# Performance work log

Measured on AMD Instinct MI355X. Metric: run time of the kernel, lower is better.

The kernel has to match this reference:

```python
import jax, jax.numpy as jnp
import numpy as np

B, L, H, W, C = 2, 32, 16, 16, 32  # L must equal channels for the view() to be consistent
CH = L  # conv channel count


def setup_inputs() -> dict:
    key = jax.random.key(0)
    k1, k2, k3, k4, k5 = jax.random.split(key, 5)
    return {
        "inputs": jax.random.normal(k1, (B, L, H, W, C), dtype=jnp.float32),
        "W1": jax.random.normal(k2, (CH // 2, CH), dtype=jnp.float32) * 0.1,
        "b1": jax.random.normal(k3, (CH // 2,), dtype=jnp.float32) * 0.1,
        "W2": jax.random.normal(k4, (CH, CH), dtype=jnp.float32) * 0.1,
        "b2": jax.random.normal(k5, (CH,), dtype=jnp.float32) * 0.1,
        "gamma": jnp.ones((1,), dtype=jnp.float32),
    }


def reference(inputs, W1, b1, W2, b2, gamma):
    b, l, h, w, c = inputs.shape
    n = l * h * w  # flattened 'spatial' positions after the (buggy-but-faithful) reshape
    # conv1x1 over dim-1 (torch Conv3d treats dim-1 as channels)
    x1 = jnp.einsum('ol,blhwc->bohwc', W1, inputs) + b1[None, :, None, None, None]
    # permute (0,4,1,2,3) then view(b, c//2, l*h*w)
    x1 = jnp.transpose(x1, (0, 4, 1, 2, 3)).reshape(b, c // 2, n)
    # attn[b, i, j] = sum_k x1[b, k, i] * x1[b, k, j]; softmax over last dim
    attn = jax.nn.softmax(jnp.einsum('bki,bkj->bij', x1, x1), axis=-1)  # [b, n, n]
    x2 = jnp.einsum('ol,blhwc->bohwc', W2, inputs) + b2[None, :, None, None, None]
    x2 = jnp.transpose(x2, (0, 4, 1, 2, 3)).reshape(b, c, n)
    # x2 @ attn^T : out[b, c, i] = sum_j x2[b, c, j] * attn[b, i, j]
    out = jnp.einsum('bcj,bij->bci', x2, attn)
    out = jnp.transpose(out.reshape(b, c, l, h, w), (0, 2, 3, 4, 1))
    return out * gamma + inputs
```

## Files before the change

kernel.cpp:

```cpp
#include <hip/hip_runtime.h>
#include <hip/hip_bf16.h>
#include <math.h>

typedef __bf16 bf16x8 __attribute__((ext_vector_type(8)));
typedef __bf16 bf16x4v __attribute__((ext_vector_type(4)));
typedef short  s16x4  __attribute__((ext_vector_type(4)));
typedef float  floatx16 __attribute__((ext_vector_type(16)));

#define KQ_ELEMS (2 * 8192 * 16)
#define OACC_OFF 1572864
#define ACC_FLOATS (16384 * 32 + 16384)
#define SQRT_LOG2E 1.2011224087864498f
#define LSPLIT 4

__global__ __launch_bounds__(256) void proj_kernel(
    const float* __restrict__ in, const float* __restrict__ W1,
    const float* __restrict__ b1, const float* __restrict__ W2,
    const float* __restrict__ b2,
    __hip_bfloat16* __restrict__ Kq, __hip_bfloat16* __restrict__ Vswz,
    float* __restrict__ acc0)
{
    __shared__ float Xs[32][32];
    __shared__ float W1s[16 * 32];
    __shared__ float W2s[32 * 32];
    const int t = threadIdx.x;
    const int bid = blockIdx.x;
    const int b = bid >> 8;
    const int hw = bid & 255;

    {
        int gid = bid * 256 + t;
        *(float4*)(acc0 + (size_t)gid * 4) = make_float4(0.f, 0.f, 0.f, 0.f);
        if (gid < 4096)
            *(float4*)(acc0 + 524288 + (size_t)gid * 4) = make_float4(0.f, 0.f, 0.f, 0.f);
    }

    {
        int l = t >> 3, cs = (t & 7) * 4;
        float4 v = *(const float4*)(in + (((size_t)b * 32 + l) * 256 + hw) * 32 + cs);
        *(float4*)&Xs[l][cs] = v;
    }
    if (t < 128) *(float4*)&W1s[t * 4] = *(const float4*)(W1 + t * 4);
    *(float4*)&W2s[t * 4] = *(const float4*)(W2 + t * 4);
    __syncthreads();

    const int c = t & 31;
    const int g = t >> 5;

#pragma unroll
    for (int oo = 0; oo < 2; ++oo) {
        int o = g * 2 + oo;
        float acc = b1[o];
#pragma unroll
        for (int l = 0; l < 32; ++l) acc += W1s[o * 32 + l] * Xs[l][c];
        int k = c >> 1;
        int i = (c & 1) * 4096 + o * 256 + hw;
        Kq[((size_t)b * 8192 + i) * 16 + k] = __float2bfloat16(acc * SQRT_LOG2E);
    }
#pragma unroll
    for (int oo = 0; oo < 4; ++oo) {
        int o = g * 4 + oo;
        float acc = b2[o];
#pragma unroll
        for (int l = 0; l < 32; ++l) acc += W2s[o * 32 + l] * Xs[l][c];
        int j = o * 256 + hw;
        int jt = j >> 5, rem = j & 31;
        int gg = rem >> 3, h = (rem >> 2) & 1, idx = rem & 3;
        Vswz[(size_t)b * 262144 + jt * 1024 + gg * 256 + h * 128 + c * 4 + idx] =
            __float2bfloat16(acc);
    }
}

__global__ __launch_bounds__(256) void flash_kernel(
    const __hip_bfloat16* __restrict__ Kq, const __hip_bfloat16* __restrict__ Vswz,
    float* __restrict__ Oacc, float* __restrict__ Lacc)
{
    const int t = threadIdx.x;
    const int lane = t & 63;
    const int wv = t >> 6;
    const int m = lane & 31;
    const int h = lane >> 5;

    const int bid = blockIdx.x;
    const int s = bid & 15;
    const int itile = (bid >> LSPLIT) & 63;
    const int b = bid >> (LSPLIT + 6);
    const int i0 = itile * 128 + wv * 32;
    const int niter = 512 >> 5;
    const int jt0 = s * niter;

    const __hip_bfloat16* Kb = Kq + (size_t)b * 8192 * 16;
    const __hip_bfloat16* Vb = Vswz + (size_t)b * 262144 + h * 128 + m * 4;

    const bf16x8 bq = *(const bf16x8*)(Kb + (size_t)(i0 + m) * 16 + h * 8);

    floatx16 oa = {}, ob = {};
    float2 l01 = {0.f, 0.f}, l23 = {0.f, 0.f};

    bf16x8 ak = *(const bf16x8*)(Kb + (size_t)(jt0 * 32 + m) * 16 + h * 8);
    s16x4 vf0 = *(const s16x4*)(Vb + (size_t)jt0 * 1024 + 0);
    s16x4 vf1 = *(const s16x4*)(Vb + (size_t)jt0 * 1024 + 256);
    s16x4 vf2 = *(const s16x4*)(Vb + (size_t)jt0 * 1024 + 512);
    s16x4 vf3 = *(const s16x4*)(Vb + (size_t)jt0 * 1024 + 768);

    for (int it = 0; it < niter; ++it) {
        const int jtn = jt0 + (it + 1 < niter ? it + 1 : it);
        bf16x8 ak_n = *(const bf16x8*)(Kb + (size_t)(jtn * 32 + m) * 16 + h * 8);
        s16x4 vn0 = *(const s16x4*)(Vb + (size_t)jtn * 1024 + 0);
        s16x4 vn1 = *(const s16x4*)(Vb + (size_t)jtn * 1024 + 256);
        s16x4 vn2 = *(const s16x4*)(Vb + (size_t)jtn * 1024 + 512);
        s16x4 vn3 = *(const s16x4*)(Vb + (size_t)jtn * 1024 + 768);

        floatx16 sc = __builtin_amdgcn_mfma_f32_32x32x16_bf16(ak, bq, (floatx16){}, 0, 0, 0);

#pragma unroll
        for (int g = 0; g < 4; ++g) {
            bf16x4v pb;
            float e0 = __builtin_amdgcn_exp2f(sc[4 * g + 0]);
            float e1 = __builtin_amdgcn_exp2f(sc[4 * g + 1]);
            float e2 = __builtin_amdgcn_exp2f(sc[4 * g + 2]);
            float e3 = __builtin_amdgcn_exp2f(sc[4 * g + 3]);
            l01.x += e0; l01.y += e1; l23.x += e2; l23.y += e3;
            pb[0] = (__bf16)e0; pb[1] = (__bf16)e1; pb[2] = (__bf16)e2; pb[3] = (__bf16)e3;
            s16x4 vf = (g == 0) ? vf0 : (g == 1) ? vf1 : (g == 2) ? vf2 : vf3;
            if (g < 2)
                oa = __builtin_amdgcn_mfma_f32_32x32x8bf16_1k(
                         __builtin_bit_cast(s16x4, pb), vf, oa, 0, 0, 0);
            else
                ob = __builtin_amdgcn_mfma_f32_32x32x8bf16_1k(
                         __builtin_bit_cast(s16x4, pb), vf, ob, 0, 0, 0);
        }
        ak = ak_n; vf0 = vn0; vf1 = vn1; vf2 = vn2; vf3 = vn3;
    }

    oa = oa + ob;
    float l = (l01.x + l01.y) + (l23.x + l23.y);
    l += __shfl_xor(l, 32);

#pragma unroll
    for (int r = 0; r < 16; ++r) {
        int iloc = (r & 3) + 8 * (r >> 2) + 4 * h;
        size_t row = (size_t)b * 8192 + i0 + iloc;
        unsafeAtomicAdd(&Oacc[row * 32 + m], oa[r]);
    }
    if (h == 0)
        unsafeAtomicAdd(&Lacc[(size_t)b * 8192 + i0 + m], l);
}

__global__ __launch_bounds__(256) void finalize_kernel(
    const float* __restrict__ Oacc, const float* __restrict__ Lacc,
    const float* __restrict__ in, const float* __restrict__ gamma,
    float* __restrict__ out)
{
    const int t = threadIdx.x;
    const int c = t & 31;
    const size_t row = (size_t)blockIdx.x * 8 + (t >> 5);
    size_t idx = row * 32 + c;
    out[idx] = (Oacc[idx] / Lacc[row]) * gamma[0] + in[idx];
}

extern "C" void kernel_launch(void* const* d_in, const int* in_sizes, int n_in,
                              void* d_out, int out_size, void* d_ws, size_t ws_size,
                              hipStream_t stream) {
    const float* in = (const float*)d_in[0];
    const float* W1 = (const float*)d_in[1];
    const float* b1 = (const float*)d_in[2];
    const float* W2 = (const float*)d_in[3];
    const float* b2 = (const float*)d_in[4];
    const float* gamma = (const float*)d_in[5];
    float* out = (float*)d_out;

    __hip_bfloat16* Kq = (__hip_bfloat16*)d_ws;
    __hip_bfloat16* Vswz = Kq + KQ_ELEMS;
    float* Oacc = (float*)((char*)d_ws + OACC_OFF);
    float* Lacc = Oacc + 16384 * 32;

    proj_kernel<<<512, 256, 0, stream>>>(in, W1, b1, W2, b2, Kq, Vswz, Oacc);
    flash_kernel<<<2 * 64 * (1 << LSPLIT), 256, 0, stream>>>(Kq, Vswz, Oacc, Lacc);
    finalize_kernel<<<2048, 256, 0, stream>>>(Oacc, Lacc, in, gamma, out);
}
```

Before: 112.3 us.

## Compute softmax row sums via MFMA with ones, halve key split, unroll by two

The softmax denominator is now accumulated by an extra MFMA that multiplies the bf16 probabilities by a ones matrix, replacing per-lane scalar adds and a cross-lane shuffle. The key-dimension split drops from 16 to 8 chunks, so each block iterates longer and issues fewer atomics. The loop is unrolled by two with double-buffered fragment loads, fp32-to-bf16 conversion uses a packed builtin when the compiler provides one, and occupancy is hinted via launch bounds. The extra MFMA per group adds matrix-unit work, and the row sums now come from bf16-rounded probabilities, which slightly changes numerics.

Measured after the change: 117.8 us. 4.9% more time.

```diff
diff --git a/kernel.cpp b/kernel.cpp
--- a/kernel.cpp
+++ b/kernel.cpp
@@ -3,15 +3,15 @@
 #include <math.h>
 
 typedef __bf16 bf16x8 __attribute__((ext_vector_type(8)));
-typedef __bf16 bf16x4v __attribute__((ext_vector_type(4)));
+typedef __bf16 bf16x2 __attribute__((ext_vector_type(2)));
+typedef short  s16x2  __attribute__((ext_vector_type(2)));
 typedef short  s16x4  __attribute__((ext_vector_type(4)));
 typedef float  floatx16 __attribute__((ext_vector_type(16)));
 
 #define KQ_ELEMS (2 * 8192 * 16)
 #define OACC_OFF 1572864
-#define ACC_FLOATS (16384 * 32 + 16384)
 #define SQRT_LOG2E 1.2011224087864498f
-#define LSPLIT 4
+#define LSPLIT 3
 
 __global__ __launch_bounds__(256) void proj_kernel(
     const float* __restrict__ in, const float* __restrict__ W1,
@@ -71,7 +71,9 @@
     }
 }
 
-__global__ __launch_bounds__(256) void flash_kernel(
+struct Frags { bf16x8 ak; s16x4 v0, v1, v2, v3; };
+
+__global__ __launch_bounds__(256, 4) void flash_kernel(
     const __hip_bfloat16* __restrict__ Kq, const __hip_bfloat16* __restrict__ Vswz,
     float* __restrict__ Oacc, float* __restrict__ Lacc)
 {
@@ -82,60 +84,69 @@
     const int h = lane >> 5;
 
     const int bid = blockIdx.x;
-    const int s = bid & 15;
+    const int s = bid & ((1 << LSPLIT) - 1);
     const int itile = (bid >> LSPLIT) & 63;
     const int b = bid >> (LSPLIT + 6);
     const int i0 = itile * 128 + wv * 32;
-    const int niter = 512 >> 5;
+    const int niter = (8192 >> LSPLIT) >> 5;
     const int jt0 = s * niter;
 
     const __hip_bfloat16* Kb = Kq + (size_t)b * 8192 * 16;
     const __hip_bfloat16* Vb = Vswz + (size_t)b * 262144 + h * 128 + m * 4;
 
     const bf16x8 bq = *(const bf16x8*)(Kb + (size_t)(i0 + m) * 16 + h * 8);
+    const s16x4 vones = {(short)0x3F80, (short)0x3F80, (short)0x3F80, (short)0x3F80};
 
-    floatx16 oa = {}, ob = {};
-    float2 l01 = {0.f, 0.f}, l23 = {0.f, 0.f};
+    floatx16 oa = {}, ob = {}, lacc = {};
 
-    bf16x8 ak = *(const bf16x8*)(Kb + (size_t)(jt0 * 32 + m) * 16 + h * 8);
-    s16x4 vf0 = *(const s16x4*)(Vb + (size_t)jt0 * 1024 + 0);
-    s16x4 vf1 = *(const s16x4*)(Vb + (size_t)jt0 * 1024 + 256);
-    s16x4 vf2 = *(const s16x4*)(Vb + (size_t)jt0 * 1024 + 512);
-    s16x4 vf3 = *(const s16x4*)(Vb + (size_t)jt0 * 1024 + 768);
+    auto load = [&](int jt) {
+        Frags f;
+        f.ak = *(const bf16x8*)(Kb + (size_t)(jt * 32 + m) * 16 + h * 8);
+        f.v0 = *(const s16x4*)(Vb + (size_t)jt * 1024 + 0);
+        f.v1 = *(const s16x4*)(Vb + (size_t)jt * 1024 + 256);
+        f.v2 = *(const s16x4*)(Vb + (size_t)jt * 1024 + 512);
+        f.v3 = *(const s16x4*)(Vb + (size_t)jt * 1024 + 768);
+        return f;
+    };
 
-    for (int it = 0; it < niter; ++it) {
-        const int jtn = jt0 + (it + 1 < niter ? it + 1 : it);
-        bf16x8 ak_n = *(const bf16x8*)(Kb + (size_t)(jtn * 32 + m) * 16 + h * 8);
-        s16x4 vn0 = *(const s16x4*)(Vb + (size_t)jtn * 1024 + 0);
-        s16x4 vn1 = *(const s16x4*)(Vb + (size_t)jtn * 1024 + 256);
-        s16x4 vn2 = *(const s16x4*)(Vb + (size_t)jtn * 1024 + 512);
-        s16x4 vn3 = *(const s16x4*)(Vb + (size_t)jtn * 1024 + 768);
-
-        floatx16 sc = __builtin_amdgcn_mfma_f32_32x32x16_bf16(ak, bq, (floatx16){}, 0, 0, 0);
-
+    auto tile = [&](const Frags& f) {
+        floatx16 sc = __builtin_amdgcn_mfma_f32_32x32x16_bf16(f.ak, bq, (floatx16){}, 0, 0, 0);
 #pragma unroll
         for (int g = 0; g < 4; ++g) {
-            bf16x4v pb;
             float e0 = __builtin_amdgcn_exp2f(sc[4 * g + 0]);
             float e1 = __builtin_amdgcn_exp2f(sc[4 * g + 1]);
             float e2 = __builtin_amdgcn_exp2f(sc[4 * g + 2]);
             float e3 = __builtin_amdgcn_exp2f(sc[4 * g + 3]);
-            l01.x += e0; l01.y += e1; l23.x += e2; l23.y += e3;
-            pb[0] = (__bf16)e0; pb[1] = (__bf16)e1; pb[2] = (__bf16)e2; pb[3] = (__bf16)e3;
-            s16x4 vf = (g == 0) ? vf0 : (g == 1) ? vf1 : (g == 2) ? vf2 : vf3;
+#if defined(__has_builtin) && __has_builtin(__builtin_amdgcn_cvt_pk_bf16_f32)
+            bf16x2 plo = __builtin_amdgcn_cvt_pk_bf16_f32(e0, e1);
+            bf16x2 phi = __builtin_amdgcn_cvt_pk_bf16_f32(e2, e3);
+#else
+            bf16x2 plo = {(__bf16)e0, (__bf16)e1};
+            bf16x2 phi = {(__bf16)e2, (__bf16)e3};
+#endif
+            s16x2 lo = __builtin_bit_cast(s16x2, plo);
+            s16x2 hi = __builtin_bit_cast(s16x2, phi);
+            s16x4 pb = {lo[0], lo[1], hi[0], hi[1]};
+            s16x4 vf = (g == 0) ? f.v0 : (g == 1) ? f.v1 : (g == 2) ? f.v2 : f.v3;
             if (g < 2)
-                oa = __builtin_amdgcn_mfma_f32_32x32x8bf16_1k(
-                         __builtin_bit_cast(s16x4, pb), vf, oa, 0, 0, 0);
+                oa = __builtin_amdgcn_mfma_f32_32x32x8bf16_1k(pb, vf, oa, 0, 0, 0);
             else
-                ob = __builtin_amdgcn_mfma_f32_32x32x8bf16_1k(
-                         __builtin_bit_cast(s16x4, pb), vf, ob, 0, 0, 0);
+                ob = __builtin_amdgcn_mfma_f32_32x32x8bf16_1k(pb, vf, ob, 0, 0, 0);
+            lacc = __builtin_amdgcn_mfma_f32_32x32x8bf16_1k(pb, vones, lacc, 0, 0, 0);
         }
-        ak = ak_n; vf0 = vn0; vf1 = vn1; vf2 = vn2; vf3 = vn3;
+    };
+
+    Frags A = load(jt0);
+    for (int it = 0; it < niter; it += 2) {
+        int jb = it + 1 < niter ? jt0 + it + 1 : jt0 + niter - 1;
+        int ja = it + 2 < niter ? jt0 + it + 2 : jt0 + niter - 1;
+        Frags B = load(jb);
+        tile(A);
+        A = load(ja);
+        tile(B);
     }
 
     oa = oa + ob;
-    float l = (l01.x + l01.y) + (l23.x + l23.y);
-    l += __shfl_xor(l, 32);
 
 #pragma unroll
     for (int r = 0; r < 16; ++r) {
@@ -143,8 +154,13 @@
         size_t row = (size_t)b * 8192 + i0 + iloc;
         unsafeAtomicAdd(&Oacc[row * 32 + m], oa[r]);
     }
-    if (h == 0)
-        unsafeAtomicAdd(&Lacc[(size_t)b * 8192 + i0 + m], l);
+    if (m == 0) {
+#pragma unroll
+        for (int r = 0; r < 16; ++r) {
+            int iloc = (r & 3) + 8 * (r >> 2) + 4 * h;
+            unsafeAtomicAdd(&Lacc[(size_t)b * 8192 + i0 + iloc], lacc[r]);
+        }
+    }
 }
 
 __global__ __launch_bounds__(256) void finalize_kernel(
```
